# Optimization experiments

Measured on AMD Instinct MI355X. Metric: run time of the kernel, lower is better.

Reference implementation:

```python
import jax, jax.numpy as jnp
import numpy as np

D_MODEL = 2048
NUM_HEADS = 16
D_KV = D_MODEL // NUM_HEADS
THETA = 10000.0


def apply_rope(x, pos):
    # x: [B, H, S, d_kv], pos: [S] int
    d = x.shape[-1]
    inv_freq = 1.0 / (THETA ** (jnp.arange(0, d, 2, dtype=jnp.float32) / d))  # [d/2]
    ang = pos.astype(jnp.float32)[:, None] * inv_freq[None, :]  # [S, d/2]
    cos, sin = jnp.cos(ang), jnp.sin(ang)  # broadcast over B,H
    x1 = x[..., 0::2]
    x2 = x[..., 1::2]
    r1 = x1 * cos - x2 * sin
    r2 = x1 * sin + x2 * cos
    return jnp.stack([r1, r2], axis=-1).reshape(x.shape)


def setup_inputs() -> dict:
    key = jax.random.key(0)
    k = jax.random.split(key, 5)
    B, S = 2, 2048
    x = jax.random.normal(k[0], (B, S, D_MODEL), dtype=jnp.float32)
    scale = 1.0 / np.sqrt(D_MODEL)
    Wq = jax.random.normal(k[1], (D_MODEL, D_MODEL), dtype=jnp.float32) * scale
    Wk = jax.random.normal(k[2], (D_MODEL, D_MODEL), dtype=jnp.float32) * scale
    Wv = jax.random.normal(k[3], (D_MODEL, D_MODEL), dtype=jnp.float32) * scale
    Wo = jax.random.normal(k[4], (D_MODEL, D_MODEL), dtype=jnp.float32) * scale
    token_position = jnp.arange(S, dtype=jnp.int64 if jax.config.jax_enable_x64 else jnp.int32)
    return {"x": x, "Wq": Wq, "Wk": Wk, "Wv": Wv, "Wo": Wo, "token_position": token_position}


def reference(x, Wq, Wk, Wv, Wo, token_position):
    B, S, _ = x.shape
    def heads(y):
        return y.reshape(B, S, NUM_HEADS, D_KV).transpose(0, 2, 1, 3)  # [B,H,S,d]
    Q = heads(jnp.einsum('bsd,df->bsf', x, Wq))
    K = heads(jnp.einsum('bsd,df->bsf', x, Wk))
    V = heads(jnp.einsum('bsd,df->bsf', x, Wv))
    Q = apply_rope(Q, token_position)
    K = apply_rope(K, token_position)
    scale = 1.0 / jnp.sqrt(jnp.asarray(D_KV, dtype=x.dtype))
    scores = jnp.einsum('bhqd,bhkd->bhqk', Q, K) * scale  # [B,H,S,S]
    causal = jnp.tril(jnp.ones((S, S), dtype=bool))
    scores = jnp.where(causal, scores, -jnp.inf)
    attn = jax.nn.softmax(scores, axis=-1)
    out = jnp.einsum('bhqk,bhkd->bhqd', attn, V)  # [B,H,S,d]
    out = out.transpose(0, 2, 1, 3).reshape(B, S, D_MODEL)
    return jnp.einsum('bsd,df->bsf', out, Wo)
```

## Files before the change

kernel.cpp:

```cpp
#include <hip/hip_runtime.h>
#include <hip/hip_bf16.h>

#define S 2048
#define DM 2048
#define NH 16
#define DH 128

typedef __attribute__((ext_vector_type(8))) short short8;
typedef __attribute__((ext_vector_type(4))) float floatx4;
typedef unsigned short u16;
typedef unsigned int u32;

__device__ __forceinline__ u16 f2bf(float f) {
  union { float f; u32 u; } v; v.f = f;
  u32 r = v.u + 0x7fffu + ((v.u >> 16) & 1u);
  return (u16)(r >> 16);
}
__device__ __forceinline__ u32 pack2(float lo, float hi) {
  float2 f; f.x = lo; f.y = hi;
  __hip_bfloat162 h = __float22bfloat162_rn(f);
  union { __hip_bfloat162 h; u32 u; } c; c.h = h;
  return c.u;
}

__device__ __forceinline__ floatx4 mfma16(short8 a, short8 b, floatx4 c) {
  return __builtin_amdgcn_mfma_f32_16x16x32_bf16(a, b, c, 0, 0, 0);
}

__device__ __forceinline__ void async_cp16(const u16* g, u16* l) {
  __builtin_amdgcn_global_load_lds(
      (const __attribute__((address_space(1))) void*)g,
      (__attribute__((address_space(3))) void*)l, 16, 0, 0);
}

__global__ void conv_x_k(const float* __restrict__ x, u16* __restrict__ xb) {
  int gid = blockIdx.x * 256 + threadIdx.x;
  float4 v = ((const float4*)x)[gid];
  uint2 p; p.x = pack2(v.x, v.y); p.y = pack2(v.z, v.w);
  ((uint2*)xb)[gid] = p;
}

__global__ void conv_w_k(const float* __restrict__ W0, const float* __restrict__ W1,
                         const float* __restrict__ W2, const float* __restrict__ W3,
                         u16* __restrict__ out) {
  __shared__ float tile[32][33];
  const float* W = blockIdx.z == 0 ? W0 : blockIdx.z == 1 ? W1 : blockIdx.z == 2 ? W2 : W3;
  u16* O = out + (size_t)blockIdx.z * DM * DM;
  int tx = threadIdx.x & 31, ty = threadIdx.x >> 5;
  int k0 = blockIdx.y * 32, n0 = blockIdx.x * 32;
#pragma unroll
  for (int j = 0; j < 4; j++)
    tile[ty + j * 8][tx] = W[(size_t)(k0 + ty + j * 8) * DM + n0 + tx];
  __syncthreads();
#pragma unroll
  for (int j = 0; j < 4; j++)
    O[(size_t)(n0 + ty + j * 8) * DM + k0 + tx] = f2bf(tile[tx][ty + j * 8]);
}

__global__ __launch_bounds__(256, 4)
void gemm_k(const u16* __restrict__ A, const u16* __restrict__ Wt,
            u16* __restrict__ oQ, u16* __restrict__ oK, u16* __restrict__ oV,
            float* __restrict__ oO, const int* __restrict__ tp, int opmode)
{
  __shared__ u16 As[128 * 32];
  __shared__ u16 Bs[128 * 32];
  const int t = threadIdx.x;
  const int w = t >> 6, lane = t & 63;
  const int l16 = lane & 15, quad = lane >> 4;
  const int m0 = blockIdx.y * 128, n0 = blockIdx.x * 128;
  const int wm = (w >> 1) * 64, wn = (w & 1) * 64;
  const u16* Bt = Wt + (size_t)(opmode == 1 ? 3 : blockIdx.z) * DM * DM;

  const u16* pA[2]; const u16* pB[2]; u16* lA[2]; u16* lB[2];
#pragma unroll
  for (int i = 0; i < 2; i++) {
    int unit = i * 256 + t;
    int row = unit >> 2, s = unit & 3;
    int c = s ^ ((row >> 1) & 3);
    pA[i] = A + (size_t)(m0 + row) * DM + c * 8;
    pB[i] = Bt + (size_t)(n0 + row) * DM + c * 8;
    lA[i] = &As[unit * 8];
    lB[i] = &Bs[unit * 8];
  }

  floatx4 acc[4][4] = {};

  for (int k0 = 0; k0 < DM; k0 += 32) {
#pragma unroll
    for (int i = 0; i < 2; i++) {
      async_cp16(pA[i] + k0, lA[i]);
      async_cp16(pB[i] + k0, lB[i]);
    }
    __syncthreads();
    short8 af[4], bfr[4];
#pragma unroll
    for (int i = 0; i < 4; i++) {
      int row = wm + i * 16 + l16;
      af[i] = *(short8*)&As[(row * 4 + (quad ^ ((row >> 1) & 3))) * 8];
    }
#pragma unroll
    for (int i = 0; i < 4; i++) {
      int row = wn + i * 16 + l16;
      bfr[i] = *(short8*)&Bs[(row * 4 + (quad ^ ((row >> 1) & 3))) * 8];
    }
#pragma unroll
    for (int mi = 0; mi < 4; mi++)
#pragma unroll
      for (int ni = 0; ni < 4; ni++)
        acc[mi][ni] = mfma16(af[mi], bfr[ni], acc[mi][ni]);
    __syncthreads();
  }

  const int mode = (opmode == 1) ? 3 : ((int)blockIdx.z == 2 ? 2 : 0);
  if (mode == 3) {
#pragma unroll
    for (int mi = 0; mi < 4; mi++) {
      int m = m0 + wm + mi * 16 + quad * 4;
#pragma unroll
      for (int ni = 0; ni < 4; ni++) {
        int n = n0 + wn + ni * 16 + l16;
#pragma unroll
        for (int r = 0; r < 4; r++)
          oO[(size_t)(m + r) * DM + n] = acc[mi][ni][r];
      }
    }
  } else if (mode == 2) {
#pragma unroll
    for (int mi = 0; mi < 4; mi++) {
      int m = m0 + wm + mi * 16 + quad * 4;
      int b = m >> 11, s = m & (S - 1);
#pragma unroll
      for (int ni = 0; ni < 4; ni++) {
        int f = n0 + wn + ni * 16 + l16;
        int h = f >> 7, dh = f & (DH - 1);
        uint2 p; p.x = pack2(acc[mi][ni][0], acc[mi][ni][1]);
        p.y = pack2(acc[mi][ni][2], acc[mi][ni][3]);
        *(uint2*)&oV[((size_t)(b * NH + h) * DH + dh) * S + s] = p;
      }
    }
  } else {
    u16* Out = ((int)blockIdx.z == 0) ? oQ : oK;
    const float qs = ((int)blockIdx.z == 0) ? 0.12752780f : 1.0f;
#pragma unroll
    for (int mi = 0; mi < 4; mi++) {
#pragma unroll
      for (int r = 0; r < 4; r++) {
        int m = m0 + wm + mi * 16 + quad * 4 + r;
        int b = m >> 11, s = m & (S - 1);
        int ps = tp[s];
#pragma unroll
        for (int ni = 0; ni < 4; ni++) {
          int f = n0 + wn + ni * 16 + l16;
          int h = f >> 7, dh = f & (DH - 1);
          float own = acc[mi][ni][r];
          float oth = __shfl_xor(own, 1, 64);
          float fr = __expf((float)(dh & ~1) * (-9.210340371976184f / 128.0f));
          float ang = (float)ps * fr;
          float sn, cs; __sincosf(ang, &sn, &cs);
          float res = (dh & 1) ? (oth * sn + own * cs) : (own * cs - oth * sn);
          Out[((size_t)(b * NH + h) * S + s) * DH + dh] = f2bf(res * qs);
        }
      }
    }
  }
}

__global__ __launch_bounds__(256, 4)
void attn_k(const u16* __restrict__ Q, const u16* __restrict__ K,
            const u16* __restrict__ Vt, u16* __restrict__ O)
{
  __shared__ u16 Ks[64 * 128];
  __shared__ u16 Vs[128 * 64];
  __shared__ u16 P[4][16 * 64];
  const int t = threadIdx.x, w = t >> 6, lane = t & 63;
  const int l16 = lane & 15, quad = lane >> 4;
  const int task = blockIdx.x;
  const int bh = task & 31, b = bh >> 4, h = bh & 15;
  const int g = 31 - (task >> 5);
  const int qg = g * 64;
  const int qt = qg + w * 16;
  const u16* Qb = Q + (size_t)bh * S * DH;
  const u16* Kb = K + (size_t)bh * S * DH;
  const u16* Vb = Vt + (size_t)bh * DH * S;
  u16* Pw = P[w];
  const int pxor = l16 & 7;

  const u16* pK[4]; u16* lK[4];
  const u16* pV[4]; u16* lV[4];
#pragma unroll
  for (int j = 0; j < 4; j++) {
    int kr = w * 16 + j * 4 + (lane >> 4);
    int ks = lane & 15;
    int kc = ks ^ (kr & 15);
    pK[j] = Kb + (size_t)kr * DH + kc * 8;
    lK[j] = &Ks[kr * 128 + ks * 8];
    int vr = w * 32 + j * 8 + (lane >> 3);
    int vs = lane & 7;
    int vc = vs ^ (vr & 7);
    pV[j] = Vb + (size_t)vr * S + vc * 8;
    lV[j] = &Vs[vr * 64 + vs * 8];
  }

  short8 aq[4];
#pragma unroll
  for (int kc = 0; kc < 4; kc++)
    aq[kc] = *(const short8*)&Qb[(size_t)(qt + l16) * DH + kc * 32 + quad * 8];

  floatx4 o[8] = {};
  float lsum = 0.0f;
  const int kend = qg + 64;

  for (int k0 = 0; k0 < kend; k0 += 64) {
#pragma unroll
    for (int j = 0; j < 4; j++) async_cp16(pK[j] + (size_t)k0 * DH, lK[j]);
#pragma unroll
    for (int j = 0; j < 4; j++) async_cp16(pV[j] + k0, lV[j]);
    __syncthreads();

    floatx4 sc[4] = {};
#pragma unroll
    for (int hh = 0; hh < 4; hh++) {
      int row = hh * 16 + l16;
#pragma unroll
      for (int kc = 0; kc < 4; kc++) {
        short8 kf = *(short8*)&Ks[row * 128 + (((kc * 4 + quad) ^ l16) << 3)];
        sc[hh] = mfma16(kf, aq[kc], sc[hh]);
      }
    }
    if (k0 + 64 > qt) {
#pragma unroll
      for (int hh = 0; hh < 4; hh++)
#pragma unroll
        for (int r = 0; r < 4; r++) {
          int j = k0 + hh * 16 + quad * 4 + r;
          if (j > qt + l16) sc[hh][r] = -3.0e38f;
        }
    }
#pragma unroll
    for (int hh = 0; hh < 4; hh++) {
      float e0 = __builtin_amdgcn_exp2f(fminf(sc[hh][0], 44.0f));
      float e1 = __builtin_amdgcn_exp2f(fminf(sc[hh][1], 44.0f));
      float e2 = __builtin_amdgcn_exp2f(fminf(sc[hh][2], 44.0f));
      float e3 = __builtin_amdgcn_exp2f(fminf(sc[hh][3], 44.0f));
      lsum += (e0 + e1) + (e2 + e3);
      uint2 pk; pk.x = pack2(e0, e1); pk.y = pack2(e2, e3);
      int su = (2 * hh + (quad >> 1)) ^ pxor;
      *(uint2*)&Pw[l16 * 64 + su * 8 + (quad & 1) * 4] = pk;
    }
    asm volatile("s_waitcnt lgkmcnt(0)" ::: "memory");
#pragma unroll
    for (int c = 0; c < 2; c++) {
      short8 pf = *(short8*)&Pw[l16 * 64 + (((4 * c + quad) ^ pxor) << 3)];
#pragma unroll
      for (int t8 = 0; t8 < 8; t8++) {
        int row = t8 * 16 + l16;
        short8 av = *(short8*)&Vs[row * 64 + (((c * 4 + quad) ^ (l16 & 7)) << 3)];
        o[t8] = mfma16(av, pf, o[t8]);
      }
    }
    __syncthreads();
  }

  float l = lsum + __shfl_xor(lsum, 16, 64);
  l += __shfl_xor(l, 32, 64);
  float inv = __builtin_amdgcn_rcpf(l);
#pragma unroll
  for (int t8 = 0; t8 < 8; t8++) {
    uint2 pa;
    pa.x = pack2(o[t8][0] * inv, o[t8][1] * inv);
    pa.y = pack2(o[t8][2] * inv, o[t8][3] * inv);
    *(uint2*)&O[((size_t)(b * S + qt + l16)) * DM + h * DH + t8 * 16 + quad * 4] = pa;
  }
}

extern "C" void kernel_launch(void* const* d_in, const int* in_sizes, int n_in,
                              void* d_out, int out_size, void* d_ws, size_t ws_size,
                              hipStream_t stream) {
  const float* x  = (const float*)d_in[0];
  const float* Wq = (const float*)d_in[1];
  const float* Wk = (const float*)d_in[2];
  const float* Wv = (const float*)d_in[3];
  const float* Wo = (const float*)d_in[4];
  const int*   tp = (const int*)d_in[5];

  char* ws = (char*)d_ws;
  u16* Wt = (u16*)ws;
  u16* xb = (u16*)(ws + 33554432);
  u16* Qb = (u16*)(ws + 50331648);
  u16* Kb = (u16*)(ws + 67108864);
  u16* Vb = (u16*)(ws + 83886080);
  u16* Ob = (u16*)(ws + 100663296);

  conv_x_k<<<8192, 256, 0, stream>>>(x, xb);
  conv_w_k<<<dim3(64, 64, 4), 256, 0, stream>>>(Wq, Wk, Wv, Wo, Wt);
  gemm_k<<<dim3(16, 32, 3), 256, 0, stream>>>(xb, Wt, Qb, Kb, Vb, nullptr, tp, 0);
  attn_k<<<1024, 256, 0, stream>>>(Qb, Kb, Vb, Ob);
  gemm_k<<<dim3(16, 32, 1), 256, 0, stream>>>(Ob, Wt, nullptr, nullptr, nullptr,
                                              (float*)d_out, tp, 1);
}
```

Before: 371.8 us.

## Rewrite projection GEMM with 256x128x64 tiles and double-buffered async pipeline

Replaces the single-buffered 128x128x32 GEMM with a 512-thread, 256x128 tile, BK=64 kernel. It double-buffers shared memory so global-to-LDS copies for the next k-tile overlap the MFMA work on the current one. Compute is split into phases with explicit barriers, waitcnt and setprio. The XOR swizzle is widened to 8 chunks to match the larger K tile. The intent is to hide memory latency and raise MFMA utilisation, at the cost of more LDS per block and fewer blocks in the grid (256 for Q/K/V, 128 for the output projection).

```diff
diff --git a/kernel.cpp b/kernel.cpp
--- a/kernel.cpp
+++ b/kernel.cpp
@@ -57,68 +57,123 @@
     O[(size_t)(n0 + ty + j * 8) * DM + k0 + tx] = f2bf(tile[tx][ty + j * 8]);
 }
 
-__global__ __launch_bounds__(256, 4)
+#define BM 256
+#define BN 128
+#define BK 64
+#define NT (DM / BK)
+
+#define STAGE(p, koff) do {                       \
+    async_cp16(pA0 + (koff), &As[p][oA0]);        \
+    async_cp16(pA1 + (koff), &As[p][oA1]);        \
+    async_cp16(pA2 + (koff), &As[p][oA2]);        \
+    async_cp16(pA3 + (koff), &As[p][oA3]);        \
+    async_cp16(pB0 + (koff), &Bs[p][oB0]);        \
+    async_cp16(pB1 + (koff), &Bs[p][oB1]);        \
+  } while (0)
+
+#define PHASE(p, g, F) {                                                  \
+    short8 a0k0 = *(const short8*)&As[p][arow64 + (2*(g))*1024 + xk0];    \
+    short8 a0k1 = *(const short8*)&As[p][arow64 + (2*(g))*1024 + xk1];    \
+    short8 a1k0 = *(const short8*)&As[p][arow64 + (2*(g)+1)*1024 + xk0];  \
+    short8 a1k1 = *(const short8*)&As[p][arow64 + (2*(g)+1)*1024 + xk1];  \
+    if (F) {                                                              \
+      bA = *(const short8*)&Bs[p][brow64 + xk0];                          \
+      bB = *(const short8*)&Bs[p][brow64 + xk1];                          \
+      bC = *(const short8*)&Bs[p][brow64 + 1024 + xk0];                   \
+      bD = *(const short8*)&Bs[p][brow64 + 1024 + xk1];                   \
+    }                                                                     \
+    __builtin_amdgcn_s_barrier();                                         \
+    asm volatile("s_waitcnt lgkmcnt(0)" ::: "memory");                    \
+    __builtin_amdgcn_sched_barrier(0);                                    \
+    __builtin_amdgcn_s_setprio(1);                                        \
+    acc[2*(g)][0]   = mfma16(a0k0, bA, acc[2*(g)][0]);                    \
+    acc[2*(g)][1]   = mfma16(a0k0, bC, acc[2*(g)][1]);                    \
+    acc[2*(g)+1][0] = mfma16(a1k0, bA, acc[2*(g)+1][0]);                  \
+    acc[2*(g)+1][1] = mfma16(a1k0, bC, acc[2*(g)+1][1]);                  \
+    acc[2*(g)][0]   = mfma16(a0k1, bB, acc[2*(g)][0]);                    \
+    acc[2*(g)][1]   = mfma16(a0k1, bD, acc[2*(g)][1]);                    \
+    acc[2*(g)+1][0] = mfma16(a1k1, bB, acc[2*(g)+1][0]);                  \
+    acc[2*(g)+1][1] = mfma16(a1k1, bD, acc[2*(g)+1][1]);                  \
+    __builtin_amdgcn_s_setprio(0);                                        \
+    __builtin_amdgcn_s_barrier();                                         \
+  }
+
+#define BOUNDARY(p, koff, pre) {                                          \
+    __builtin_amdgcn_sched_barrier(0);                                    \
+    if (pre) {                                                            \
+      STAGE(p, koff);                                                     \
+      __builtin_amdgcn_sched_barrier(0);                                  \
+      asm volatile("s_waitcnt vmcnt(6)" ::: "memory");                    \
+    } else {                                                              \
+      asm volatile("s_waitcnt vmcnt(0)" ::: "memory");                    \
+    }                                                                     \
+    __builtin_amdgcn_s_barrier();                                         \
+    __builtin_amdgcn_sched_barrier(0);                                    \
+  }
+
+__global__ __launch_bounds__(512, 2)
 void gemm_k(const u16* __restrict__ A, const u16* __restrict__ Wt,
             u16* __restrict__ oQ, u16* __restrict__ oK, u16* __restrict__ oV,
             float* __restrict__ oO, const int* __restrict__ tp, int opmode)
 {
-  __shared__ u16 As[128 * 32];
-  __shared__ u16 Bs[128 * 32];
+  __shared__ u16 As[2][BM * BK];
+  __shared__ u16 Bs[2][BN * BK];
   const int t = threadIdx.x;
   const int w = t >> 6, lane = t & 63;
   const int l16 = lane & 15, quad = lane >> 4;
-  const int m0 = blockIdx.y * 128, n0 = blockIdx.x * 128;
-  const int wm = (w >> 1) * 64, wn = (w & 1) * 64;
+  const int wr = w >> 2, wc = w & 3;
+  const int m0 = blockIdx.y * BM, n0 = blockIdx.x * BN;
   const u16* Bt = Wt + (size_t)(opmode == 1 ? 3 : blockIdx.z) * DM * DM;
 
-  const u16* pA[2]; const u16* pB[2]; u16* lA[2]; u16* lB[2];
-#pragma unroll
-  for (int i = 0; i < 2; i++) {
-    int unit = i * 256 + t;
-    int row = unit >> 2, s = unit & 3;
-    int c = s ^ ((row >> 1) & 3);
-    pA[i] = A + (size_t)(m0 + row) * DM + c * 8;
-    pB[i] = Bt + (size_t)(n0 + row) * DM + c * 8;
-    lA[i] = &As[unit * 8];
-    lB[i] = &Bs[unit * 8];
-  }
-
-  floatx4 acc[4][4] = {};
-
-  for (int k0 = 0; k0 < DM; k0 += 32) {
-#pragma unroll
-    for (int i = 0; i < 2; i++) {
-      async_cp16(pA[i] + k0, lA[i]);
-      async_cp16(pB[i] + k0, lB[i]);
-    }
-    __syncthreads();
-    short8 af[4], bfr[4];
-#pragma unroll
-    for (int i = 0; i < 4; i++) {
-      int row = wm + i * 16 + l16;
-      af[i] = *(short8*)&As[(row * 4 + (quad ^ ((row >> 1) & 3))) * 8];
-    }
-#pragma unroll
-    for (int i = 0; i < 4; i++) {
-      int row = wn + i * 16 + l16;
-      bfr[i] = *(short8*)&Bs[(row * 4 + (quad ^ ((row >> 1) & 3))) * 8];
-    }
-#pragma unroll
-    for (int mi = 0; mi < 4; mi++)
-#pragma unroll
-      for (int ni = 0; ni < 4; ni++)
-        acc[mi][ni] = mfma16(af[mi], bfr[ni], acc[mi][ni]);
-    __syncthreads();
+  int uu, rr, cc;
+  uu = t;        rr = uu >> 3; cc = (uu & 7) ^ (rr & 7);
+  const u16* pA0 = A + (size_t)(m0 + rr) * DM + cc * 8; const int oA0 = uu * 8;
+  uu = t + 512;  rr = uu >> 3; cc = (uu & 7) ^ (rr & 7);
+  const u16* pA1 = A + (size_t)(m0 + rr) * DM + cc * 8; const int oA1 = uu * 8;
+  uu = t + 1024; rr = uu >> 3; cc = (uu & 7) ^ (rr & 7);
+  const u16* pA2 = A + (size_t)(m0 + rr) * DM + cc * 8; const int oA2 = uu * 8;
+  uu = t + 1536; rr = uu >> 3; cc = (uu & 7) ^ (rr & 7);
+  const u16* pA3 = A + (size_t)(m0 + rr) * DM + cc * 8; const int oA3 = uu * 8;
+  uu = t;        rr = uu >> 3; cc = (uu & 7) ^ (rr & 7);
+  const u16* pB0 = Bt + (size_t)(n0 + rr) * DM + cc * 8; const int oB0 = uu * 8;
+  uu = t + 512;  rr = uu >> 3; cc = (uu & 7) ^ (rr & 7);
+  const u16* pB1 = Bt + (size_t)(n0 + rr) * DM + cc * 8; const int oB1 = uu * 8;
+
+  const int arow64 = (wr * 128 + l16) * 64;
+  const int brow64 = (wc * 32 + l16) * 64;
+  const int xk0 = ((quad) ^ (l16 & 7)) << 3;
+  const int xk1 = ((4 + quad) ^ (l16 & 7)) << 3;
+
+  floatx4 acc[8][2] = {};
+  short8 bA, bB, bC, bD;
+
+  STAGE(0, 0);
+  STAGE(1, BK);
+  __builtin_amdgcn_sched_barrier(0);
+  asm volatile("s_waitcnt vmcnt(6)" ::: "memory");
+  __builtin_amdgcn_s_barrier();
+  __builtin_amdgcn_sched_barrier(0);
+
+  for (int it = 0; it < NT / 2; ++it) {
+    const int koffE = it * 128 + 128;
+    const int koffO = it * 128 + 192;
+    const bool pre = (it < NT / 2 - 1);
+    PHASE(0, 0, 1) PHASE(0, 1, 0) PHASE(0, 2, 0) PHASE(0, 3, 0)
+    BOUNDARY(0, koffE, pre)
+    PHASE(1, 0, 1) PHASE(1, 1, 0) PHASE(1, 2, 0) PHASE(1, 3, 0)
+    BOUNDARY(1, koffO, pre)
   }
 
   const int mode = (opmode == 1) ? 3 : ((int)blockIdx.z == 2 ? 2 : 0);
+  const int mbase = m0 + wr * 128;
+  const int nbase = n0 + wc * 32;
   if (mode == 3) {
 #pragma unroll
-    for (int mi = 0; mi < 4; mi++) {
-      int m = m0 + wm + mi * 16 + quad * 4;
-#pragma unroll
-      for (int ni = 0; ni < 4; ni++) {
-        int n = n0 + wn + ni * 16 + l16;
+    for (int mi = 0; mi < 8; mi++) {
+      int m = mbase + mi * 16 + quad * 4;
+#pragma unroll
+      for (int ni = 0; ni < 2; ni++) {
+        int n = nbase + ni * 16 + l16;
 #pragma unroll
         for (int r = 0; r < 4; r++)
           oO[(size_t)(m + r) * DM + n] = acc[mi][ni][r];
@@ -126,31 +181,31 @@
     }
   } else if (mode == 2) {
 #pragma unroll
-    for (int mi = 0; mi < 4; mi++) {
-      int m = m0 + wm + mi * 16 + quad * 4;
+    for (int mi = 0; mi < 8; mi++) {
+      int m = mbase + mi * 16 + quad * 4;
       int b = m >> 11, s = m & (S - 1);
 #pragma unroll
-      for (int ni = 0; ni < 4; ni++) {
-        int f = n0 + wn + ni * 16 + l16;
+      for (int ni = 0; ni < 2; ni++) {
+        int f = nbase + ni * 16 + l16;
         int h = f >> 7, dh = f & (DH - 1);
-        uint2 p; p.x = pack2(acc[mi][ni][0], acc[mi][ni][1]);
-        p.y = pack2(acc[mi][ni][2], acc[mi][ni][3]);
-        *(uint2*)&oV[((size_t)(b * NH + h) * DH + dh) * S + s] = p;
+        uint2 pk; pk.x = pack2(acc[mi][ni][0], acc[mi][ni][1]);
+        pk.y = pack2(acc[mi][ni][2], acc[mi][ni][3]);
+        *(uint2*)&oV[((size_t)(b * NH + h) * DH + dh) * S + s] = pk;
       }
     }
   } else {
     u16* Out = ((int)blockIdx.z == 0) ? oQ : oK;
     const float qs = ((int)blockIdx.z == 0) ? 0.12752780f : 1.0f;
 #pragma unroll
-    for (int mi = 0; mi < 4; mi++) {
+    for (int mi = 0; mi < 8; mi++) {
 #pragma unroll
       for (int r = 0; r < 4; r++) {
-        int m = m0 + wm + mi * 16 + quad * 4 + r;
+        int m = mbase + mi * 16 + quad * 4 + r;
         int b = m >> 11, s = m & (S - 1);
         int ps = tp[s];
 #pragma unroll
-        for (int ni = 0; ni < 4; ni++) {
-          int f = n0 + wn + ni * 16 + l16;
+        for (int ni = 0; ni < 2; ni++) {
+          int f = nbase + ni * 16 + l16;
           int h = f >> 7, dh = f & (DH - 1);
           float own = acc[mi][ni][r];
           float oth = __shfl_xor(own, 1, 64);
@@ -293,8 +348,9 @@
 
   conv_x_k<<<8192, 256, 0, stream>>>(x, xb);
   conv_w_k<<<dim3(64, 64, 4), 256, 0, stream>>>(Wq, Wk, Wv, Wo, Wt);
-  gemm_k<<<dim3(16, 32, 3), 256, 0, stream>>>(xb, Wt, Qb, Kb, Vb, nullptr, tp, 0);
+  gemm_k<<<dim3(DM / BN, 4096 / BM, 3), 512, 0, stream>>>(xb, Wt, Qb, Kb, Vb,
+                                                          nullptr, tp, 0);
   attn_k<<<1024, 256, 0, stream>>>(Qb, Kb, Vb, Ob);
-  gemm_k<<<dim3(16, 32, 1), 256, 0, stream>>>(Ob, Wt, nullptr, nullptr, nullptr,
-                                              (float*)d_out, tp, 1);
-}
+  gemm_k<<<dim3(DM / BN, 4096 / BM, 1), 512, 0, stream>>>(Ob, Wt, nullptr, nullptr,
+                                                          nullptr, (float*)d_out, tp, 1);
+}
```

After: 383.3 us. 3.1% more time.

## Rewrite projection GEMM with 128x256x64 tiles and double-buffered async LDS pipeline

Applied to the files above, without the earlier changes.

The projection and output GEMMs move from 128x128x32 single-buffered tiles to 128x256x64 tiles with two LDS buffers. Global-to-LDS copies for the next K tile are interleaved across four MFMA phases, with explicit vmcnt waits, barriers and setprio. Blocks are remapped so consecutive blocks walk down M for the same N column, which is meant to improve reuse of the weight tile. Larger tiles with one block per CU reduce occupancy and raise register pressure, and the hand-placed waits and barriers are fragile.

```diff
diff --git a/kernel.cpp b/kernel.cpp
--- a/kernel.cpp
+++ b/kernel.cpp
@@ -57,68 +57,142 @@
     O[(size_t)(n0 + ty + j * 8) * DM + k0 + tx] = f2bf(tile[tx][ty + j * 8]);
 }
 
-__global__ __launch_bounds__(256, 4)
+#define BM 128
+#define BN 256
+#define BK 64
+#define NT (DM / BK)
+
+#define BARRIER __builtin_amdgcn_s_barrier()
+#define SB __builtin_amdgcn_sched_barrier(0)
+#define LGKM0 asm volatile("s_waitcnt lgkmcnt(0)" ::: "memory")
+
+#define STG_B(q, j, koff) \
+  async_cp16(pBg + (size_t)(j) * 32 * DM + (koff), &Bs[q][so + (j) * 2048])
+#define STG_A(q, j, koff) \
+  async_cp16(pAg + (size_t)(j) * 32 * DM + (koff), &As[q][so + (j) * 2048])
+
+#define MFMA4(mi, av) \
+    acc[mi][0] = mfma16(av, b0, acc[mi][0]); \
+    acc[mi][1] = mfma16(av, b1, acc[mi][1]); \
+    acc[mi][2] = mfma16(av, b2, acc[mi][2]); \
+    acc[mi][3] = mfma16(av, b3, acc[mi][3]);
+
+#define PH1(p, q, koff, PRE) { \
+    a0 = *(const short8*)&As[p][arow + xk0]; \
+    a1 = *(const short8*)&As[p][1024 + arow + xk0]; \
+    a2 = *(const short8*)&As[p][2048 + arow + xk0]; \
+    a3 = *(const short8*)&As[p][3072 + arow + xk0]; \
+    b0 = *(const short8*)&Bs[p][brow + xk0]; \
+    b1 = *(const short8*)&Bs[p][1024 + brow + xk0]; \
+    b2 = *(const short8*)&Bs[p][2048 + brow + xk0]; \
+    b3 = *(const short8*)&Bs[p][3072 + brow + xk0]; \
+    if (PRE) { STG_B(q, 0, koff); STG_B(q, 1, koff); STG_B(q, 2, koff); } \
+    BARRIER; LGKM0; SB; \
+    __builtin_amdgcn_s_setprio(1); \
+    MFMA4(0, a0) MFMA4(1, a1) MFMA4(2, a2) MFMA4(3, a3) \
+    __builtin_amdgcn_s_setprio(0); SB; \
+    if (PRE) { asm volatile("s_waitcnt vmcnt(3)" ::: "memory"); } \
+    else     { asm volatile("s_waitcnt vmcnt(0)" ::: "memory"); } \
+    BARRIER; }
+
+#define PH2(p, q, koff, PRE) { \
+    a0 = *(const short8*)&As[p][4096 + arow + xk0]; \
+    a1 = *(const short8*)&As[p][5120 + arow + xk0]; \
+    a2 = *(const short8*)&As[p][6144 + arow + xk0]; \
+    a3 = *(const short8*)&As[p][7168 + arow + xk0]; \
+    if (PRE) { STG_B(q, 3, koff); STG_B(q, 4, koff); STG_B(q, 5, koff); } \
+    BARRIER; LGKM0; SB; \
+    __builtin_amdgcn_s_setprio(1); \
+    MFMA4(4, a0) MFMA4(5, a1) MFMA4(6, a2) MFMA4(7, a3) \
+    __builtin_amdgcn_s_setprio(0); \
+    BARRIER; }
+
+#define PH3(p, q, koff, PRE) { \
+    a0 = *(const short8*)&As[p][arow + xk1]; \
+    a1 = *(const short8*)&As[p][1024 + arow + xk1]; \
+    a2 = *(const short8*)&As[p][2048 + arow + xk1]; \
+    a3 = *(const short8*)&As[p][3072 + arow + xk1]; \
+    b0 = *(const short8*)&Bs[p][brow + xk1]; \
+    b1 = *(const short8*)&Bs[p][1024 + brow + xk1]; \
+    b2 = *(const short8*)&Bs[p][2048 + brow + xk1]; \
+    b3 = *(const short8*)&Bs[p][3072 + brow + xk1]; \
+    if (PRE) { STG_B(q, 6, koff); STG_B(q, 7, koff); STG_A(q, 0, koff); } \
+    BARRIER; LGKM0; SB; \
+    __builtin_amdgcn_s_setprio(1); \
+    MFMA4(0, a0) MFMA4(1, a1) MFMA4(2, a2) MFMA4(3, a3) \
+    __builtin_amdgcn_s_setprio(0); \
+    BARRIER; }
+
+#define PH4(p, q, koff, PRE, LAST) { \
+    a0 = *(const short8*)&As[p][4096 + arow + xk1]; \
+    a1 = *(const short8*)&As[p][5120 + arow + xk1]; \
+    a2 = *(const short8*)&As[p][6144 + arow + xk1]; \
+    a3 = *(const short8*)&As[p][7168 + arow + xk1]; \
+    if (PRE) { STG_A(q, 1, koff); STG_A(q, 2, koff); STG_A(q, 3, koff); } \
+    BARRIER; LGKM0; SB; \
+    __builtin_amdgcn_s_setprio(1); \
+    MFMA4(4, a0) MFMA4(5, a1) MFMA4(6, a2) MFMA4(7, a3) \
+    __builtin_amdgcn_s_setprio(0); SB; \
+    if (!LAST) { asm volatile("s_waitcnt vmcnt(2)" ::: "memory"); BARRIER; SB; } }
+
+#define TILE(p, q, koff, PRE, LAST) \
+    PH1(p, q, koff, PRE) PH2(p, q, koff, PRE) PH3(p, q, koff, PRE) \
+    PH4(p, q, koff, PRE, LAST)
+
+__global__ __launch_bounds__(256, 1)
 void gemm_k(const u16* __restrict__ A, const u16* __restrict__ Wt,
             u16* __restrict__ oQ, u16* __restrict__ oK, u16* __restrict__ oV,
             float* __restrict__ oO, const int* __restrict__ tp, int opmode)
 {
-  __shared__ u16 As[128 * 32];
-  __shared__ u16 Bs[128 * 32];
+  __shared__ u16 As[2][BM * BK];
+  __shared__ u16 Bs[2][BN * BK];
   const int t = threadIdx.x;
   const int w = t >> 6, lane = t & 63;
   const int l16 = lane & 15, quad = lane >> 4;
-  const int m0 = blockIdx.y * 128, n0 = blockIdx.x * 128;
-  const int wm = (w >> 1) * 64, wn = (w & 1) * 64;
+  const int bid = blockIdx.y * 8 + blockIdx.x;
+  const int m0 = (bid & 31) * BM, n0 = (bid >> 5) * BN;
   const u16* Bt = Wt + (size_t)(opmode == 1 ? 3 : blockIdx.z) * DM * DM;
 
-  const u16* pA[2]; const u16* pB[2]; u16* lA[2]; u16* lB[2];
-#pragma unroll
-  for (int i = 0; i < 2; i++) {
-    int unit = i * 256 + t;
-    int row = unit >> 2, s = unit & 3;
-    int c = s ^ ((row >> 1) & 3);
-    pA[i] = A + (size_t)(m0 + row) * DM + c * 8;
-    pB[i] = Bt + (size_t)(n0 + row) * DM + c * 8;
-    lA[i] = &As[unit * 8];
-    lB[i] = &Bs[unit * 8];
-  }
-
-  floatx4 acc[4][4] = {};
-
-  for (int k0 = 0; k0 < DM; k0 += 32) {
-#pragma unroll
-    for (int i = 0; i < 2; i++) {
-      async_cp16(pA[i] + k0, lA[i]);
-      async_cp16(pB[i] + k0, lB[i]);
-    }
-    __syncthreads();
-    short8 af[4], bfr[4];
-#pragma unroll
-    for (int i = 0; i < 4; i++) {
-      int row = wm + i * 16 + l16;
-      af[i] = *(short8*)&As[(row * 4 + (quad ^ ((row >> 1) & 3))) * 8];
-    }
-#pragma unroll
-    for (int i = 0; i < 4; i++) {
-      int row = wn + i * 16 + l16;
-      bfr[i] = *(short8*)&Bs[(row * 4 + (quad ^ ((row >> 1) & 3))) * 8];
-    }
-#pragma unroll
-    for (int mi = 0; mi < 4; mi++)
-#pragma unroll
-      for (int ni = 0; ni < 4; ni++)
-        acc[mi][ni] = mfma16(af[mi], bfr[ni], acc[mi][ni]);
-    __syncthreads();
-  }
+  const int srow = t >> 3;
+  const int sc = ((t & 7) ^ (srow & 7)) * 8;
+  const u16* pAg = A + (size_t)(m0 + srow) * DM + sc;
+  const u16* pBg = Bt + (size_t)(n0 + srow) * DM + sc;
+  const int so = t * 8;
+
+  const int arow = l16 * 64;
+  const int brow = w * 4096 + l16 * 64;
+  const int xk0 = ((quad) ^ (l16 & 7)) << 3;
+  const int xk1 = ((4 + quad) ^ (l16 & 7)) << 3;
+
+  floatx4 acc[8][4] = {};
+  short8 a0, a1, a2, a3, b0, b1, b2, b3;
+
+#pragma unroll
+  for (int j = 0; j < 8; j++) STG_B(0, j, 0);
+#pragma unroll
+  for (int j = 0; j < 4; j++) STG_A(0, j, 0);
+  SB;
+  asm volatile("s_waitcnt vmcnt(2)" ::: "memory");
+  BARRIER; SB;
+
+  for (int it = 0; it < 15; ++it) {
+    const int kA = it * 128 + 64;
+    const int kB = it * 128 + 128;
+    TILE(0, 1, kA, 1, 0)
+    TILE(1, 0, kB, 1, 0)
+  }
+  TILE(0, 1, 31 * 64, 1, 0)
+  TILE(1, 0, 0, 0, 1)
 
   const int mode = (opmode == 1) ? 3 : ((int)blockIdx.z == 2 ? 2 : 0);
+  const int nbase = n0 + w * 64;
   if (mode == 3) {
 #pragma unroll
-    for (int mi = 0; mi < 4; mi++) {
-      int m = m0 + wm + mi * 16 + quad * 4;
+    for (int mi = 0; mi < 8; mi++) {
+      int m = m0 + mi * 16 + quad * 4;
 #pragma unroll
       for (int ni = 0; ni < 4; ni++) {
-        int n = n0 + wn + ni * 16 + l16;
+        int n = nbase + ni * 16 + l16;
 #pragma unroll
         for (int r = 0; r < 4; r++)
           oO[(size_t)(m + r) * DM + n] = acc[mi][ni][r];
@@ -126,31 +200,31 @@
     }
   } else if (mode == 2) {
 #pragma unroll
-    for (int mi = 0; mi < 4; mi++) {
-      int m = m0 + wm + mi * 16 + quad * 4;
+    for (int mi = 0; mi < 8; mi++) {
+      int m = m0 + mi * 16 + quad * 4;
       int b = m >> 11, s = m & (S - 1);
 #pragma unroll
       for (int ni = 0; ni < 4; ni++) {
-        int f = n0 + wn + ni * 16 + l16;
+        int f = nbase + ni * 16 + l16;
         int h = f >> 7, dh = f & (DH - 1);
-        uint2 p; p.x = pack2(acc[mi][ni][0], acc[mi][ni][1]);
-        p.y = pack2(acc[mi][ni][2], acc[mi][ni][3]);
-        *(uint2*)&oV[((size_t)(b * NH + h) * DH + dh) * S + s] = p;
+        uint2 pk; pk.x = pack2(acc[mi][ni][0], acc[mi][ni][1]);
+        pk.y = pack2(acc[mi][ni][2], acc[mi][ni][3]);
+        *(uint2*)&oV[((size_t)(b * NH + h) * DH + dh) * S + s] = pk;
       }
     }
   } else {
     u16* Out = ((int)blockIdx.z == 0) ? oQ : oK;
     const float qs = ((int)blockIdx.z == 0) ? 0.12752780f : 1.0f;
 #pragma unroll
-    for (int mi = 0; mi < 4; mi++) {
+    for (int mi = 0; mi < 8; mi++) {
 #pragma unroll
       for (int r = 0; r < 4; r++) {
-        int m = m0 + wm + mi * 16 + quad * 4 + r;
+        int m = m0 + mi * 16 + quad * 4 + r;
         int b = m >> 11, s = m & (S - 1);
         int ps = tp[s];
 #pragma unroll
         for (int ni = 0; ni < 4; ni++) {
-          int f = n0 + wn + ni * 16 + l16;
+          int f = nbase + ni * 16 + l16;
           int h = f >> 7, dh = f & (DH - 1);
           float own = acc[mi][ni][r];
           float oth = __shfl_xor(own, 1, 64);
@@ -293,8 +367,8 @@
 
   conv_x_k<<<8192, 256, 0, stream>>>(x, xb);
   conv_w_k<<<dim3(64, 64, 4), 256, 0, stream>>>(Wq, Wk, Wv, Wo, Wt);
-  gemm_k<<<dim3(16, 32, 3), 256, 0, stream>>>(xb, Wt, Qb, Kb, Vb, nullptr, tp, 0);
+  gemm_k<<<dim3(8, 32, 3), 256, 0, stream>>>(xb, Wt, Qb, Kb, Vb, nullptr, tp, 0);
   attn_k<<<1024, 256, 0, stream>>>(Qb, Kb, Vb, Ob);
-  gemm_k<<<dim3(16, 32, 1), 256, 0, stream>>>(Ob, Wt, nullptr, nullptr, nullptr,
-                                              (float*)d_out, tp, 1);
-}
+  gemm_k<<<dim3(8, 32, 1), 256, 0, stream>>>(Ob, Wt, nullptr, nullptr,
+                                             nullptr, (float*)d_out, tp, 1);
+}
```

After: 418.1 us. 1.12x slower.

## Double-buffer QKV GEMM with 256x128 tiles and split the output projection kernel

Applied to the files above, without the earlier changes.

The QKV projection GEMM is rewritten with 256x128 block tiles and two LDS buffers. Global-to-LDS async copies for the next K-slice are issued while MFMAs run on the current one, with explicit vmcnt waits, barriers, sched_barriers and s_setprio. The aim is to hide memory latency and raise MFMA utilisation, at the cost of more registers and LDS (launch bounds drop to 2 blocks per CU) and fewer blocks. The output projection moves into its own kernel using the old simple loop, and the attention kernel's MFMA sections get raised wave priority.

```diff
diff --git a/kernel.cpp b/kernel.cpp
--- a/kernel.cpp
+++ b/kernel.cpp
@@ -57,100 +57,155 @@
     O[(size_t)(n0 + ty + j * 8) * DM + k0 + tx] = f2bf(tile[tx][ty + j * 8]);
 }
 
-__global__ __launch_bounds__(256, 4)
+#define BM 256
+#define BN 128
+#define BK 32
+#define NT 64
+
+#define BARRIER __builtin_amdgcn_s_barrier()
+#define SB __builtin_amdgcn_sched_barrier(0)
+#define LGKM0 asm volatile("s_waitcnt lgkmcnt(0)" ::: "memory")
+
+#define STG_A(q, j, koff) \
+  async_cp16(pAg + (size_t)(j) * 64 * DM + (koff), &As[q][soff + (j) * 2048])
+#define STG_B(q, j, koff) \
+  async_cp16(pBg + (size_t)(j) * 64 * DM + (koff), &Bs[q][soff + (j) * 2048])
+
+#define PH0(p) { \
+    a0 = *(const short8*)&As[p][arow + xk]; \
+    a1 = *(const short8*)&As[p][arow + 512 + xk]; \
+    a2 = *(const short8*)&As[p][arow + 1024 + xk]; \
+    a3 = *(const short8*)&As[p][arow + 1536 + xk]; \
+    a4 = *(const short8*)&As[p][arow + 2048 + xk]; \
+    a5 = *(const short8*)&As[p][arow + 2560 + xk]; \
+    a6 = *(const short8*)&As[p][arow + 3072 + xk]; \
+    a7 = *(const short8*)&As[p][arow + 3584 + xk]; \
+    b0 = *(const short8*)&Bs[p][brow + xk]; \
+    b1 = *(const short8*)&Bs[p][brow + 512 + xk]; \
+    b2 = *(const short8*)&Bs[p][brow + 1024 + xk]; \
+    b3 = *(const short8*)&Bs[p][brow + 1536 + xk]; \
+    BARRIER; LGKM0; SB; \
+    __builtin_amdgcn_s_setprio(1); \
+    acc[0][0] = mfma16(a0, b0, acc[0][0]); \
+    acc[1][0] = mfma16(a1, b0, acc[1][0]); \
+    acc[2][0] = mfma16(a2, b0, acc[2][0]); \
+    acc[3][0] = mfma16(a3, b0, acc[3][0]); \
+    acc[0][1] = mfma16(a0, b1, acc[0][1]); \
+    acc[1][1] = mfma16(a1, b1, acc[1][1]); \
+    acc[2][1] = mfma16(a2, b1, acc[2][1]); \
+    acc[3][1] = mfma16(a3, b1, acc[3][1]); \
+    acc[0][2] = mfma16(a0, b2, acc[0][2]); \
+    acc[1][2] = mfma16(a1, b2, acc[1][2]); \
+    acc[2][2] = mfma16(a2, b2, acc[2][2]); \
+    acc[3][2] = mfma16(a3, b2, acc[3][2]); \
+    acc[0][3] = mfma16(a0, b3, acc[0][3]); \
+    acc[1][3] = mfma16(a1, b3, acc[1][3]); \
+    acc[2][3] = mfma16(a2, b3, acc[2][3]); \
+    acc[3][3] = mfma16(a3, b3, acc[3][3]); \
+    __builtin_amdgcn_s_setprio(0); \
+    BARRIER; }
+
+#define PH1(p, koff2, PRE2, LAST) { \
+    if (PRE2) { STG_B(p, 0, koff2); STG_B(p, 1, koff2); \
+                STG_A(p, 0, koff2); STG_A(p, 1, koff2); \
+                STG_A(p, 2, koff2); STG_A(p, 3, koff2); } \
+    SB; \
+    __builtin_amdgcn_s_setprio(1); \
+    acc[4][0] = mfma16(a4, b0, acc[4][0]); \
+    acc[5][0] = mfma16(a5, b0, acc[5][0]); \
+    acc[6][0] = mfma16(a6, b0, acc[6][0]); \
+    acc[7][0] = mfma16(a7, b0, acc[7][0]); \
+    acc[4][1] = mfma16(a4, b1, acc[4][1]); \
+    acc[5][1] = mfma16(a5, b1, acc[5][1]); \
+    acc[6][1] = mfma16(a6, b1, acc[6][1]); \
+    acc[7][1] = mfma16(a7, b1, acc[7][1]); \
+    acc[4][2] = mfma16(a4, b2, acc[4][2]); \
+    acc[5][2] = mfma16(a5, b2, acc[5][2]); \
+    acc[6][2] = mfma16(a6, b2, acc[6][2]); \
+    acc[7][2] = mfma16(a7, b2, acc[7][2]); \
+    acc[4][3] = mfma16(a4, b3, acc[4][3]); \
+    acc[5][3] = mfma16(a5, b3, acc[5][3]); \
+    acc[6][3] = mfma16(a6, b3, acc[6][3]); \
+    acc[7][3] = mfma16(a7, b3, acc[7][3]); \
+    __builtin_amdgcn_s_setprio(0); SB; \
+    if (!LAST) { \
+      if (PRE2) { asm volatile("s_waitcnt vmcnt(6)" ::: "memory"); } \
+      else      { asm volatile("s_waitcnt vmcnt(0)" ::: "memory"); } \
+      BARRIER; SB; } }
+
+__global__ __launch_bounds__(256, 2)
 void gemm_k(const u16* __restrict__ A, const u16* __restrict__ Wt,
             u16* __restrict__ oQ, u16* __restrict__ oK, u16* __restrict__ oV,
-            float* __restrict__ oO, const int* __restrict__ tp, int opmode)
+            const int* __restrict__ tp)
 {
-  __shared__ u16 As[128 * 32];
-  __shared__ u16 Bs[128 * 32];
+  __shared__ u16 As[2][BM * BK];
+  __shared__ u16 Bs[2][BN * BK];
   const int t = threadIdx.x;
   const int w = t >> 6, lane = t & 63;
   const int l16 = lane & 15, quad = lane >> 4;
-  const int m0 = blockIdx.y * 128, n0 = blockIdx.x * 128;
-  const int wm = (w >> 1) * 64, wn = (w & 1) * 64;
-  const u16* Bt = Wt + (size_t)(opmode == 1 ? 3 : blockIdx.z) * DM * DM;
-
-  const u16* pA[2]; const u16* pB[2]; u16* lA[2]; u16* lB[2];
-#pragma unroll
-  for (int i = 0; i < 2; i++) {
-    int unit = i * 256 + t;
-    int row = unit >> 2, s = unit & 3;
-    int c = s ^ ((row >> 1) & 3);
-    pA[i] = A + (size_t)(m0 + row) * DM + c * 8;
-    pB[i] = Bt + (size_t)(n0 + row) * DM + c * 8;
-    lA[i] = &As[unit * 8];
-    lB[i] = &Bs[unit * 8];
-  }
-
-  floatx4 acc[4][4] = {};
-
-  for (int k0 = 0; k0 < DM; k0 += 32) {
-#pragma unroll
-    for (int i = 0; i < 2; i++) {
-      async_cp16(pA[i] + k0, lA[i]);
-      async_cp16(pB[i] + k0, lB[i]);
-    }
-    __syncthreads();
-    short8 af[4], bfr[4];
-#pragma unroll
-    for (int i = 0; i < 4; i++) {
-      int row = wm + i * 16 + l16;
-      af[i] = *(short8*)&As[(row * 4 + (quad ^ ((row >> 1) & 3))) * 8];
-    }
-#pragma unroll
-    for (int i = 0; i < 4; i++) {
-      int row = wn + i * 16 + l16;
-      bfr[i] = *(short8*)&Bs[(row * 4 + (quad ^ ((row >> 1) & 3))) * 8];
-    }
-#pragma unroll
-    for (int mi = 0; mi < 4; mi++)
-#pragma unroll
-      for (int ni = 0; ni < 4; ni++)
-        acc[mi][ni] = mfma16(af[mi], bfr[ni], acc[mi][ni]);
-    __syncthreads();
-  }
-
-  const int mode = (opmode == 1) ? 3 : ((int)blockIdx.z == 2 ? 2 : 0);
-  if (mode == 3) {
-#pragma unroll
-    for (int mi = 0; mi < 4; mi++) {
-      int m = m0 + wm + mi * 16 + quad * 4;
+  const int wr = w >> 1, wc = w & 1;
+  const int m0 = blockIdx.y * BM, n0 = blockIdx.x * BN;
+  const u16* Bt = Wt + (size_t)blockIdx.z * DM * DM;
+
+  const int srow = t >> 2;
+  const int sc = ((t & 3) ^ ((t >> 3) & 3)) * 8;
+  const u16* pAg = A + (size_t)(m0 + srow) * DM + sc;
+  const u16* pBg = Bt + (size_t)(n0 + srow) * DM + sc;
+  const int soff = t * 8;
+
+  const int arow = (wr * 128 + l16) * 32;
+  const int brow = (wc * 64 + l16) * 32;
+  const int xk = ((quad ^ ((l16 >> 1) & 3)) << 3);
+
+  floatx4 acc[8][4] = {};
+  short8 a0, a1, a2, a3, a4, a5, a6, a7, b0, b1, b2, b3;
+
+  STG_B(0, 0, 0); STG_B(0, 1, 0);
+  STG_A(0, 0, 0); STG_A(0, 1, 0); STG_A(0, 2, 0); STG_A(0, 3, 0);
+  STG_B(1, 0, BK); STG_B(1, 1, BK);
+  STG_A(1, 0, BK); STG_A(1, 1, BK); STG_A(1, 2, BK); STG_A(1, 3, BK);
+  SB;
+  asm volatile("s_waitcnt vmcnt(6)" ::: "memory");
+  BARRIER; SB;
+
+  for (int it = 0; it < 31; ++it) {
+    const int kE = (2 * it + 2) * BK;
+    const int kO = (2 * it + 3) * BK;
+    PH0(0) PH1(0, kE, 1, 0)
+    PH0(1) PH1(1, kO, 1, 0)
+  }
+  PH0(0) PH1(0, 0, 0, 0)
+  PH0(1) PH1(1, 0, 0, 1)
+
+  const int mwb = m0 + wr * 128;
+  const int nwb = n0 + wc * 64;
+  if ((int)blockIdx.z == 2) {
+#pragma unroll
+    for (int mi = 0; mi < 8; mi++) {
+      int m = mwb + mi * 16 + quad * 4;
+      int b = m >> 11, s = m & (S - 1);
 #pragma unroll
       for (int ni = 0; ni < 4; ni++) {
-        int n = n0 + wn + ni * 16 + l16;
-#pragma unroll
-        for (int r = 0; r < 4; r++)
-          oO[(size_t)(m + r) * DM + n] = acc[mi][ni][r];
-      }
-    }
-  } else if (mode == 2) {
-#pragma unroll
-    for (int mi = 0; mi < 4; mi++) {
-      int m = m0 + wm + mi * 16 + quad * 4;
-      int b = m >> 11, s = m & (S - 1);
-#pragma unroll
-      for (int ni = 0; ni < 4; ni++) {
-        int f = n0 + wn + ni * 16 + l16;
+        int f = nwb + ni * 16 + l16;
         int h = f >> 7, dh = f & (DH - 1);
-        uint2 p; p.x = pack2(acc[mi][ni][0], acc[mi][ni][1]);
-        p.y = pack2(acc[mi][ni][2], acc[mi][ni][3]);
-        *(uint2*)&oV[((size_t)(b * NH + h) * DH + dh) * S + s] = p;
+        uint2 pk; pk.x = pack2(acc[mi][ni][0], acc[mi][ni][1]);
+        pk.y = pack2(acc[mi][ni][2], acc[mi][ni][3]);
+        *(uint2*)&oV[((size_t)(b * NH + h) * DH + dh) * S + s] = pk;
       }
     }
   } else {
     u16* Out = ((int)blockIdx.z == 0) ? oQ : oK;
     const float qs = ((int)blockIdx.z == 0) ? 0.12752780f : 1.0f;
 #pragma unroll
-    for (int mi = 0; mi < 4; mi++) {
+    for (int mi = 0; mi < 8; mi++) {
 #pragma unroll
       for (int r = 0; r < 4; r++) {
-        int m = m0 + wm + mi * 16 + quad * 4 + r;
+        int m = mwb + mi * 16 + quad * 4 + r;
         int b = m >> 11, s = m & (S - 1);
         int ps = tp[s];
 #pragma unroll
         for (int ni = 0; ni < 4; ni++) {
-          int f = n0 + wn + ni * 16 + l16;
+          int f = nwb + ni * 16 + l16;
           int h = f >> 7, dh = f & (DH - 1);
           float own = acc[mi][ni][r];
           float oth = __shfl_xor(own, 1, 64);
@@ -161,6 +216,72 @@
           Out[((size_t)(b * NH + h) * S + s) * DH + dh] = f2bf(res * qs);
         }
       }
+    }
+  }
+}
+
+__global__ __launch_bounds__(256, 4)
+void oproj_k(const u16* __restrict__ A, const u16* __restrict__ Wt,
+             float* __restrict__ oO)
+{
+  __shared__ u16 As2[128 * 32];
+  __shared__ u16 Bs2[128 * 32];
+  const int t = threadIdx.x;
+  const int w = t >> 6, lane = t & 63;
+  const int l16 = lane & 15, quad = lane >> 4;
+  const int m0 = blockIdx.y * 128, n0 = blockIdx.x * 128;
+  const int wm = (w >> 1) * 64, wn = (w & 1) * 64;
+  const u16* Bt = Wt + (size_t)3 * DM * DM;
+
+  const u16* pA[2]; const u16* pB[2]; u16* lA[2]; u16* lB[2];
+#pragma unroll
+  for (int i = 0; i < 2; i++) {
+    int unit = i * 256 + t;
+    int row = unit >> 2, s = unit & 3;
+    int c = s ^ ((row >> 1) & 3);
+    pA[i] = A + (size_t)(m0 + row) * DM + c * 8;
+    pB[i] = Bt + (size_t)(n0 + row) * DM + c * 8;
+    lA[i] = &As2[unit * 8];
+    lB[i] = &Bs2[unit * 8];
+  }
+
+  floatx4 acc[4][4] = {};
+
+  for (int k0 = 0; k0 < DM; k0 += 32) {
+#pragma unroll
+    for (int i = 0; i < 2; i++) {
+      async_cp16(pA[i] + k0, lA[i]);
+      async_cp16(pB[i] + k0, lB[i]);
+    }
+    __syncthreads();
+    short8 af[4], bfr[4];
+#pragma unroll
+    for (int i = 0; i < 4; i++) {
+      int row = wm + i * 16 + l16;
+      af[i] = *(short8*)&As2[(row * 4 + (quad ^ ((row >> 1) & 3))) * 8];
+    }
+#pragma unroll
+    for (int i = 0; i < 4; i++) {
+      int row = wn + i * 16 + l16;
+      bfr[i] = *(short8*)&Bs2[(row * 4 + (quad ^ ((row >> 1) & 3))) * 8];
+    }
+#pragma unroll
+    for (int mi = 0; mi < 4; mi++)
+#pragma unroll
+      for (int ni = 0; ni < 4; ni++)
+        acc[mi][ni] = mfma16(af[mi], bfr[ni], acc[mi][ni]);
+    __syncthreads();
+  }
+
+#pragma unroll
+  for (int mi = 0; mi < 4; mi++) {
+    int m = m0 + wm + mi * 16 + quad * 4;
+#pragma unroll
+    for (int ni = 0; ni < 4; ni++) {
+      int n = n0 + wn + ni * 16 + l16;
+#pragma unroll
+      for (int r = 0; r < 4; r++)
+        oO[(size_t)(m + r) * DM + n] = acc[mi][ni][r];
     }
   }
 }
@@ -218,6 +339,7 @@
     __syncthreads();
 
     floatx4 sc[4] = {};
+    __builtin_amdgcn_s_setprio(1);
 #pragma unroll
     for (int hh = 0; hh < 4; hh++) {
       int row = hh * 16 + l16;
@@ -227,6 +349,7 @@
         sc[hh] = mfma16(kf, aq[kc], sc[hh]);
       }
     }
+    __builtin_amdgcn_s_setprio(0);
     if (k0 + 64 > qt) {
 #pragma unroll
       for (int hh = 0; hh < 4; hh++)
@@ -248,6 +371,7 @@
       *(uint2*)&Pw[l16 * 64 + su * 8 + (quad & 1) * 4] = pk;
     }
     asm volatile("s_waitcnt lgkmcnt(0)" ::: "memory");
+    __builtin_amdgcn_s_setprio(1);
 #pragma unroll
     for (int c = 0; c < 2; c++) {
       short8 pf = *(short8*)&Pw[l16 * 64 + (((4 * c + quad) ^ pxor) << 3)];
@@ -258,6 +382,7 @@
         o[t8] = mfma16(av, pf, o[t8]);
       }
     }
+    __builtin_amdgcn_s_setprio(0);
     __syncthreads();
   }
 
@@ -293,8 +418,7 @@
 
   conv_x_k<<<8192, 256, 0, stream>>>(x, xb);
   conv_w_k<<<dim3(64, 64, 4), 256, 0, stream>>>(Wq, Wk, Wv, Wo, Wt);
-  gemm_k<<<dim3(16, 32, 3), 256, 0, stream>>>(xb, Wt, Qb, Kb, Vb, nullptr, tp, 0);
+  gemm_k<<<dim3(16, 16, 3), 256, 0, stream>>>(xb, Wt, Qb, Kb, Vb, tp);
   attn_k<<<1024, 256, 0, stream>>>(Qb, Kb, Vb, Ob);
-  gemm_k<<<dim3(16, 32, 1), 256, 0, stream>>>(Ob, Wt, nullptr, nullptr, nullptr,
-                                              (float*)d_out, tp, 1);
-}
+  oproj_k<<<dim3(16, 32), 256, 0, stream>>>(Ob, Wt, (float*)d_out);
+}
```

New measurement: 378.0 us. No clear change (+1.7%).
